# Performance work log

Measured on AMD Instinct MI355X. Metric: run time of the kernel, lower is better.

The kernel has to match this reference:

```python
import jax, jax.numpy as jnp
import numpy as np

B, N, C, D, K = 8, 4096, 64, 64, 16


def _knn_indices(features, k):
    # so topk-smallest indices match torch.cdist + topk(largest=False))
    sq = jnp.sum(features * features, axis=-1)                      # [B, N]
    d2 = sq[:, :, None] + sq[:, None, :] - 2.0 * jnp.einsum('bic,bjc->bij', features, features)
    n = features.shape[1]
    eye = jnp.eye(n, dtype=bool)[None]                              # mask self
    d2 = jnp.where(eye, jnp.inf, d2)
    _, idx = jax.lax.top_k(-d2, k)                                  # k smallest
    return idx                                                      # [B, N, k]


def setup_inputs() -> dict:
    key = jax.random.key(0)
    k0, k1, k2 = jax.random.split(key, 3)
    features = jax.random.normal(k0, (B, N, C), dtype=jnp.float32)
    W1 = jax.random.normal(k1, (2 * C, D), dtype=jnp.float32) * 0.05
    b1 = jnp.zeros((D,), dtype=jnp.float32)
    W2 = jax.random.normal(k2, (D, D), dtype=jnp.float32) * 0.05
    b2 = jnp.zeros((D,), dtype=jnp.float32)
    return {"features": features, "W1": W1, "b1": b1, "W2": W2, "b2": b2}


def reference(features, W1, b1, W2, b2):
    idx = _knn_indices(features, K)                                 # [B, N, K]
    neighbors = jax.vmap(lambda f, i: f[i])(features, idx)          # [B, N, K, C]
    central = features[:, :, None, :]                               # [B, N, 1, C]
    edge = jnp.concatenate(
        [jnp.broadcast_to(central, neighbors.shape), neighbors - central], axis=-1
    )                                                               # [B, N, K, 2C]
    h = jax.nn.gelu(edge @ W1 + b1, approximate=False)              # exact GELU (torch default)
    h = jax.nn.gelu(h @ W2 + b2, approximate=False)                 # [B, N, K, D]
    return jnp.max(h, axis=2)                                       # [B, N, D]
```

## Files before the change

kernel.cpp:

```cpp
#include <hip/hip_runtime.h>
#include <math.h>
#include <stdint.h>

#define B 8
#define N 4096
#define C 64
#define D 64
#define K 16

typedef __attribute__((ext_vector_type(8))) short short8;
typedef __attribute__((ext_vector_type(4))) float f32x4;

__device__ __forceinline__ unsigned short f2bf(float x) {
    unsigned u = __float_as_uint(x);
    unsigned r = (u + 0x7FFFu + ((u >> 16) & 1u)) >> 16;
    return (unsigned short)r;
}
__device__ __forceinline__ float bf2f(unsigned short h) {
    return __uint_as_float(((unsigned)h) << 16);
}

__device__ __forceinline__ double pack_key(float d2, unsigned idx) {
    uint2 u; u.x = idx; u.y = __float_as_uint(d2);
    return __builtin_bit_cast(double, u);
}

__global__ __launch_bounds__(256)
void prep_kernel(const float* __restrict__ F, float* __restrict__ sq,
                 unsigned short* __restrict__ HP, unsigned short* __restrict__ MP,
                 unsigned short* __restrict__ LP) {
    const int row = blockIdx.x * 256 + threadIdx.x;
    const float4* src = (const float4*)(F + (size_t)row * C);
    float4 v[16];
    #pragma unroll
    for (int q = 0; q < 16; q++) v[q] = src[q];

    {
        float r[8];
        #pragma unroll
        for (int j = 0; j < 8; j++) {
            float t = ((const float*)v)[j];
            r[j] = t * t;
        }
        #pragma unroll
        for (int m = 1; m < 8; m++) {
            #pragma unroll
            for (int j = 0; j < 8; j++) {
                float t = ((const float*)v)[8 * m + j];
                r[j] = fmaf(t, t, r[j]);
            }
        }
        sq[row] = ((r[0] + r[1]) + (r[2] + r[3])) + ((r[4] + r[5]) + (r[6] + r[7]));
    }

    uint4* dh = (uint4*)(HP + (size_t)row * C);
    uint4* dm = (uint4*)(MP + (size_t)row * C);
    uint4* dl = (uint4*)(LP + (size_t)row * C);
    #pragma unroll
    for (int c8 = 0; c8 < 8; c8++) {
        unsigned hq[4], mq[4], lq[4];
        #pragma unroll
        for (int e = 0; e < 4; e++) {
            float x0 = ((const float*)v)[c8 * 8 + 2 * e];
            float x1 = ((const float*)v)[c8 * 8 + 2 * e + 1];
            unsigned short h0 = f2bf(x0), h1 = f2bf(x1);
            float r10 = x0 - bf2f(h0), r11 = x1 - bf2f(h1);
            unsigned short m0 = f2bf(r10), m1 = f2bf(r11);
            float r20 = r10 - bf2f(m0), r21 = r11 - bf2f(m1);
            unsigned short l0 = f2bf(r20), l1 = f2bf(r21);
            hq[e] = (unsigned)h0 | ((unsigned)h1 << 16);
            mq[e] = (unsigned)m0 | ((unsigned)m1 << 16);
            lq[e] = (unsigned)l0 | ((unsigned)l1 << 16);
        }
        dh[c8] = make_uint4(hq[0], hq[1], hq[2], hq[3]);
        dm[c8] = make_uint4(mq[0], mq[1], mq[2], mq[3]);
        dl[c8] = make_uint4(lq[0], lq[1], lq[2], lq[3]);
    }
}

__device__ __forceinline__ void merge4_store(const uint64_t* __restrict__ keys,
                                             int qloc, uint64_t* __restrict__ dst) {
    const uint64_t* K0 = keys + (qloc * 4 + 0) * 16;
    const uint64_t* K1 = keys + (qloc * 4 + 1) * 16;
    const uint64_t* K2 = keys + (qloc * 4 + 2) * 16;
    const uint64_t* K3 = keys + (qloc * 4 + 3) * 16;
    int p0 = 0, p1 = 0, p2 = 0, p3 = 0;
    uint64_t h0 = K0[0], h1 = K1[0], h2 = K2[0], h3 = K3[0];
    #pragma unroll
    for (int k = 0; k < K; k++) {
        uint64_t m01 = h0 < h1 ? h0 : h1;
        uint64_t m23 = h2 < h3 ? h2 : h3;
        uint64_t mv  = m01 < m23 ? m01 : m23;
        dst[k] = mv;
        if      (mv == h0) { ++p0; h0 = (p0 < 16) ? K0[p0] : ~0ull; }
        else if (mv == h1) { ++p1; h1 = (p1 < 16) ? K1[p1] : ~0ull; }
        else if (mv == h2) { ++p2; h2 = (p2 < 16) ? K2[p2] : ~0ull; }
        else               { ++p3; h3 = (p3 < 16) ? K3[p3] : ~0ull; }
    }
}

__global__ __launch_bounds__(512, 2)
void knn_mfma_kernel(const unsigned short* __restrict__ HP,
                     const unsigned short* __restrict__ MP,
                     const unsigned short* __restrict__ LP,
                     const float* __restrict__ sqg, uint64_t* __restrict__ keysg) {
    __shared__ __align__(16) char lds[49152];

    const int s  = blockIdx.y;
    const int b  = blockIdx.z;
    const int i0 = blockIdx.x * 128;
    const int c0 = s * 2048;
    const unsigned short* Hb = HP + (size_t)b * N * C;
    const unsigned short* Mb = MP + (size_t)b * N * C;
    const unsigned short* Lb = LP + (size_t)b * N * C;
    const float* sqb = sqg + (size_t)b * N;

    const int tid = threadIdx.x;
    const int l   = tid & 63;
    const int w   = tid >> 6;

    const int lr  = tid >> 3;
    const int lq  = tid & 7;
    const int wbyte = (lr * 128 + lq * 16) ^ ((lr & 7) << 4);

    const double KMAX = __builtin_bit_cast(double, 0x7FEFFFFFFFFFFFFFull);

    uint4 ph, pm, pl;
    {
        const size_t rb = (size_t)(c0 + lr) * C + lq * 8;
        ph = *(const uint4*)(Hb + rb);
        pm = *(const uint4*)(Mb + rb);
        pl = *(const uint4*)(Lb + rb);
    }

    {
        const size_t r0 = (size_t)(i0 + lr) * C + lq * 8;
        const size_t r1 = (size_t)(i0 + 64 + lr) * C + lq * 8;
        uint4 qh0 = *(const uint4*)(Hb + r0), qh1 = *(const uint4*)(Hb + r1);
        uint4 qm0 = *(const uint4*)(Mb + r0), qm1 = *(const uint4*)(Mb + r1);
        uint4 ql0 = *(const uint4*)(Lb + r0), ql1 = *(const uint4*)(Lb + r1);
        *(uint4*)(lds +              wbyte) = qh0;
        *(uint4*)(lds +  8192      + wbyte) = qm0;
        *(uint4*)(lds + 16384      + wbyte) = ql0;
        *(uint4*)(lds + 24576      + wbyte) = qh1;
        *(uint4*)(lds + 24576+8192 + wbyte) = qm1;
        *(uint4*)(lds + 24576+16384+ wbyte) = ql1;
    }
    __syncthreads();

    const int koff = (l >> 4) * 16;
    const int swzR = (l & 7) << 4;
    const int qrow = w * 16 + (l & 15);
    const char* qbuf = lds + ((qrow >> 6) ? 24576 : 0);
    const int qr6 = qrow & 63;
    const int qb0 = (qr6 * 128 + koff) ^ swzR;
    const int qb1 = (qr6 * 128 + 64 + koff) ^ swzR;
    short8 bh0 = *(const short8*)(qbuf + qb0),         bh1 = *(const short8*)(qbuf + qb1);
    short8 bm0 = *(const short8*)(qbuf +  8192 + qb0), bm1 = *(const short8*)(qbuf +  8192 + qb1);
    short8 bl0 = *(const short8*)(qbuf + 16384 + qb0), bl1 = *(const short8*)(qbuf + 16384 + qb1);

    const float sqq   = sqb[i0 + qrow];
    const int   qglob = i0 + qrow;
    const int   crow0 = (l >> 4) * 4;
    const int   dtile = i0 + ((w >> 2) << 6);

    __syncthreads();

    *(uint4*)(lds +         wbyte) = ph;
    *(uint4*)(lds +  8192 + wbyte) = pm;
    *(uint4*)(lds + 16384 + wbyte) = pl;
    {
        const size_t rb = (size_t)(c0 + 64 + lr) * C + lq * 8;
        ph = *(const uint4*)(Hb + rb);
        pm = *(const uint4*)(Mb + rb);
        pl = *(const uint4*)(Lb + rb);
    }
    __syncthreads();

    double bd[16];
    #pragma unroll
    for (int k = 0; k < 16; k++) bd[k] = KMAX;

    for (int t = 0; t < 32; t++) {
        const int j0 = c0 + t * 64;
        char* bufA = lds + ((t & 1) ? 24576 : 0);
        char* bufB = lds + ((t & 1) ? 0 : 24576);

        if (t < 31) {
            *(uint4*)(bufB +         wbyte) = ph;
            *(uint4*)(bufB +  8192 + wbyte) = pm;
            *(uint4*)(bufB + 16384 + wbyte) = pl;
        }
        if (t < 30) {
            const size_t rb = (size_t)(j0 + 128 + lr) * C + lq * 8;
            ph = *(const uint4*)(Hb + rb);
            pm = *(const uint4*)(Mb + rb);
            pl = *(const uint4*)(Lb + rb);
        }

        float4 sqm0 = *(const float4*)(sqb + j0 +      crow0);
        float4 sqm1 = *(const float4*)(sqb + j0 + 16 + crow0);
        float4 sqm2 = *(const float4*)(sqb + j0 + 32 + crow0);
        float4 sqm3 = *(const float4*)(sqb + j0 + 48 + crow0);

        double nk[16];

        #pragma unroll
        for (int m = 0; m < 4; m++) {
            const int arow = m * 16 + (l & 15);
            const int ab0 = (arow * 128 + koff) ^ swzR;
            const int ab1 = (arow * 128 + 64 + koff) ^ swzR;
            short8 ah0 = *(const short8*)(bufA + ab0);
            short8 ah1 = *(const short8*)(bufA + ab1);
            short8 am0 = *(const short8*)(bufA + 8192 + ab0);
            short8 am1 = *(const short8*)(bufA + 8192 + ab1);
            short8 al0 = *(const short8*)(bufA + 16384 + ab0);
            short8 al1 = *(const short8*)(bufA + 16384 + ab1);

            f32x4 acc1 = {0.f, 0.f, 0.f, 0.f};
            acc1 = __builtin_amdgcn_mfma_f32_16x16x32_bf16(am0, bm0, acc1, 0, 0, 0);
            acc1 = __builtin_amdgcn_mfma_f32_16x16x32_bf16(am1, bm1, acc1, 0, 0, 0);
            acc1 = __builtin_amdgcn_mfma_f32_16x16x32_bf16(ah0, bl0, acc1, 0, 0, 0);
            acc1 = __builtin_amdgcn_mfma_f32_16x16x32_bf16(ah1, bl1, acc1, 0, 0, 0);
            acc1 = __builtin_amdgcn_mfma_f32_16x16x32_bf16(al0, bh0, acc1, 0, 0, 0);
            f32x4 acc2 = {0.f, 0.f, 0.f, 0.f};
            acc2 = __builtin_amdgcn_mfma_f32_16x16x32_bf16(al1, bh1, acc2, 0, 0, 0);
            acc2 = __builtin_amdgcn_mfma_f32_16x16x32_bf16(ah0, bm0, acc2, 0, 0, 0);
            acc2 = __builtin_amdgcn_mfma_f32_16x16x32_bf16(ah1, bm1, acc2, 0, 0, 0);
            acc2 = __builtin_amdgcn_mfma_f32_16x16x32_bf16(am0, bh0, acc2, 0, 0, 0);
            acc2 = __builtin_amdgcn_mfma_f32_16x16x32_bf16(am1, bh1, acc2, 0, 0, 0);
            f32x4 acch = {0.f, 0.f, 0.f, 0.f};
            acch = __builtin_amdgcn_mfma_f32_16x16x32_bf16(ah0, bh0, acch, 0, 0, 0);
            acch = __builtin_amdgcn_mfma_f32_16x16x32_bf16(ah1, bh1, acch, 0, 0, 0);

            float4 sqm = (m == 0) ? sqm0 : (m == 1) ? sqm1 : (m == 2) ? sqm2 : sqm3;
            #pragma unroll
            for (int r = 0; r < 4; r++) {
                float sqc = (r == 0) ? sqm.x : (r == 1) ? sqm.y : (r == 2) ? sqm.z : sqm.w;
                float gg = acch[r] + (acc1[r] + acc2[r]);
                float d2 = fmaf(-2.0f, gg, sqq + sqc);
                d2 = fmaxf(d2, 0.0f);
                nk[m * 4 + r] = pack_key(d2, (unsigned)(j0 + m * 16 + crow0 + r));
            }
        }

        if (j0 == dtile) {
            #pragma unroll
            for (int m = 0; m < 4; m++)
                #pragma unroll
                for (int r = 0; r < 4; r++)
                    if ((j0 + m * 16 + crow0 + r) == qglob) nk[m * 4 + r] = KMAX;
        }

        #pragma unroll
        for (int p = 1; p < 16; p <<= 1) {
            #pragma unroll
            for (int kk = p; kk >= 1; kk >>= 1) {
                #pragma unroll
                for (int j = kk % p; j <= 16 - 1 - kk; j += 2 * kk) {
                    #pragma unroll
                    for (int i = 0; i <= ((kk - 1 < 16 - j - kk - 1) ? kk - 1 : 16 - j - kk - 1); i++) {
                        if ((i + j) / (2 * p) == (i + j + kk) / (2 * p)) {
                            double a = nk[i + j], c2 = nk[i + j + kk];
                            nk[i + j]      = fmax(a, c2);
                            nk[i + j + kk] = fmin(a, c2);
                        }
                    }
                }
            }
        }
        #pragma unroll
        for (int i = 0; i < 16; i++) bd[i] = fmin(bd[i], nk[i]);
        #pragma unroll
        for (int j = 8; j > 0; j >>= 1) {
            #pragma unroll
            for (int i = 0; i < 16; i++) {
                int ixj = i ^ j;
                if (ixj > i) {
                    double a = bd[i], c2 = bd[ixj];
                    bd[i]   = fmin(a, c2);
                    bd[ixj] = fmax(a, c2);
                }
            }
        }

        __syncthreads();
    }

    uint64_t* keys = (uint64_t*)lds;
    if (w < 4) {
        const int qloc = w * 16 + (l & 15);
        const int base = (qloc * 4 + (l >> 4)) * 16;
        #pragma unroll
        for (int k = 0; k < 16; k++)
            keys[base + k] = __builtin_bit_cast(uint64_t, bd[k]);
    }
    __syncthreads();
    if (tid < 64)
        merge4_store(keys, tid, keysg + ((size_t)b * N + i0 + tid) * 32 + s * 16);
    __syncthreads();
    if (w >= 4) {
        const int qloc = (w - 4) * 16 + (l & 15);
        const int base = (qloc * 4 + (l >> 4)) * 16;
        #pragma unroll
        for (int k = 0; k < 16; k++)
            keys[base + k] = __builtin_bit_cast(uint64_t, bd[k]);
    }
    __syncthreads();
    if (tid < 64)
        merge4_store(keys, tid, keysg + ((size_t)b * N + i0 + 64 + tid) * 32 + s * 16);
}

__global__ __launch_bounds__(256)
void knn_merge_kernel(const uint64_t* __restrict__ keysg, int* __restrict__ knn) {
    const int q = blockIdx.x * 256 + threadIdx.x;
    const uint64_t* A  = keysg + (size_t)q * 32;
    const uint64_t* Bp = A + 16;
    int pa = 0, pb = 0;
    uint64_t ha = A[0], hb = Bp[0];
    int* dst = knn + (size_t)q * K;
    #pragma unroll
    for (int k = 0; k < K; k++) {
        uint64_t mv = ha < hb ? ha : hb;
        dst[k] = (int)(mv & 0xFFFFFFFFu);
        if (mv == ha) { ++pa; ha = (pa < 16) ? A[pa] : ~0ull; }
        else          { ++pb; hb = (pb < 16) ? Bp[pb] : ~0ull; }
    }
}

__device__ __forceinline__ float gelu_fast(float x) {
    float az = fabsf(x) * 0.70710678118654752440f;
    float t  = __builtin_amdgcn_rcpf(fmaf(0.3275911f, az, 1.0f));
    float p  = t * fmaf(t, fmaf(t, fmaf(t, fmaf(t, 1.061405429f, -1.453152027f),
                                        1.421413741f), -0.284496736f), 0.254829592f);
    float e  = p * __builtin_amdgcn_exp2f(-az * az * 1.44269504088896f);
    float g  = 0.5f * x;
    return (x >= 0.0f) ? g * (2.0f - e) : g * e;
}

#define QPW 4

__global__ __launch_bounds__(256)
void mlp_mfma_kernel(const float* __restrict__ F,
                     const unsigned short* __restrict__ HP,
                     const unsigned short* __restrict__ MP,
                     const int* __restrict__ knn,
                     const float* __restrict__ W1, const float* __restrict__ b1,
                     const float* __restrict__ W2, const float* __restrict__ b2,
                     float* __restrict__ out) {
    __shared__ __align__(16) unsigned short W1h[64 * 128];
    __shared__ __align__(16) unsigned short W1m[64 * 128];
    __shared__ __align__(16) unsigned short hbh[4][1024];
    __shared__ __align__(16) unsigned short hbm[4][1024];

    const int tid = threadIdx.x;
    const int l   = tid & 63;
    const int w   = tid >> 6;

    for (int e = tid; e < 8192; e += 256) {
        const int n = e & 63, k = e >> 6;
        const int srcrow = (k < 64) ? (64 + k) : (k - 64);
        float x = W1[srcrow * 64 + n];
        unsigned short hh = f2bf(x);
        unsigned short mm = f2bf(x - bf2f(hh));
        const int byte = (n * 256 + k * 2) ^ ((n & 15) << 4);
        *(unsigned short*)((char*)W1h + byte) = hh;
        *(unsigned short*)((char*)W1m + byte) = mm;
    }

    short8 B2h[4][2], B2m[4][2];
    float b1v[4], b2v[4];
    {
        const int n = (l & 15);
        #pragma unroll
        for (int nt = 0; nt < 4; nt++) {
            const int nn = nt * 16 + n;
            b1v[nt] = b1[nn];
            b2v[nt] = b2[nn];
            #pragma unroll
            for (int c = 0; c < 2; c++) {
                const int k0 = c * 32 + (l >> 4) * 8;
                short8 vh, vm;
                #pragma unroll
                for (int jj = 0; jj < 8; jj++) {
                    float x = W2[(k0 + jj) * 64 + nn];
                    unsigned short hh = f2bf(x);
                    vh[jj] = (short)hh;
                    vm[jj] = (short)f2bf(x - bf2f(hh));
                }
                B2h[nt][c] = vh; B2m[nt][c] = vm;
            }
        }
    }
    __syncthreads();

    const int cb   = (l >> 4) * 8;
    const int swzL = (l & 15) << 4;

    for (int jq = 0; jq < QPW; jq++) {
        const int q  = (blockIdx.x * 4 + w) * QPW + jq;
        const int b  = q >> 12;
        const int ci = q & (N - 1);
        const float*          Fb  = F  + (size_t)b * N * C;
        const unsigned short* HPb = HP + (size_t)b * N * C;
        const unsigned short* MPb = MP + (size_t)b * N * C;

        const int nb = knn[(size_t)q * K + (l & 15)];

        float4 cA0 = *(const float4*)(Fb + (size_t)ci * C + cb);
        float4 cA1 = *(const float4*)(Fb + (size_t)ci * C + cb + 4);
        float4 cB0 = *(const float4*)(Fb + (size_t)ci * C + 32 + cb);
        float4 cB1 = *(const float4*)(Fb + (size_t)ci * C + 36 + cb);
        float4 nA0 = *(const float4*)(Fb + (size_t)nb * C + cb);
        float4 nA1 = *(const float4*)(Fb + (size_t)nb * C + cb + 4);
        float4 nB0 = *(const float4*)(Fb + (size_t)nb * C + 32 + cb);
        float4 nB1 = *(const float4*)(Fb + (size_t)nb * C + 36 + cb);

        short8 ach0 = *(const short8*)(HPb + (size_t)ci * C + cb);
        short8 ach1 = *(const short8*)(HPb + (size_t)ci * C + 32 + cb);
        short8 acm0 = *(const short8*)(MPb + (size_t)ci * C + cb);
        short8 acm1 = *(const short8*)(MPb + (size_t)ci * C + 32 + cb);

        short8 adh0, adm0, adh1, adm1;
        {
            float d0[8] = {nA0.x - cA0.x, nA0.y - cA0.y, nA0.z - cA0.z, nA0.w - cA0.w,
                           nA1.x - cA1.x, nA1.y - cA1.y, nA1.z - cA1.z, nA1.w - cA1.w};
            float d1[8] = {nB0.x - cB0.x, nB0.y - cB0.y, nB0.z - cB0.z, nB0.w - cB0.w,
                           nB1.x - cB1.x, nB1.y - cB1.y, nB1.z - cB1.z, nB1.w - cB1.w};
            #pragma unroll
            for (int jj = 0; jj < 8; jj++) {
                unsigned short h0 = f2bf(d0[jj]);
                adh0[jj] = (short)h0; adm0[jj] = (short)f2bf(d0[jj] - bf2f(h0));
                unsigned short h1 = f2bf(d1[jj]);
                adh1[jj] = (short)h1; adm1[jj] = (short)f2bf(d1[jj] - bf2f(h1));
            }
        }

        #pragma unroll
        for (int nt = 0; nt < 4; nt++) {
            const int rowb = (nt * 16 + (l & 15)) * 256 + (l >> 4) * 16;
            f32x4 a1 = {0.f, 0.f, 0.f, 0.f};
            f32x4 a2 = {0.f, 0.f, 0.f, 0.f};
            #pragma unroll
            for (int kc = 0; kc < 4; kc++) {
                const int byte = (rowb + kc * 64) ^ swzL;
                short8 Bh = *(const short8*)((char*)W1h + byte);
                short8 Bm = *(const short8*)((char*)W1m + byte);
                short8 Ah = (kc == 0) ? adh0 : (kc == 1) ? adh1 : (kc == 2) ? ach0 : ach1;
                short8 Am = (kc == 0) ? adm0 : (kc == 1) ? adm1 : (kc == 2) ? acm0 : acm1;
                a1 = __builtin_amdgcn_mfma_f32_16x16x32_bf16(Ah, Bh, a1, 0, 0, 0);
                a2 = __builtin_amdgcn_mfma_f32_16x16x32_bf16(Ah, Bm, a2, 0, 0, 0);
                a2 = __builtin_amdgcn_mfma_f32_16x16x32_bf16(Am, Bh, a2, 0, 0, 0);
            }
            #pragma unroll
            for (int r = 0; r < 4; r++) {
                const int row = (l >> 4) * 4 + r;
                const int col = nt * 16 + (l & 15);
                float hv = gelu_fast(a1[r] + a2[r] + b1v[nt]);
                unsigned short hh = f2bf(hv);
                unsigned short hm = f2bf(hv - bf2f(hh));
                const int byte = (row * 128 + col * 2) ^ ((row & 7) << 4);
                *(unsigned short*)((char*)&hbh[w][0] + byte) = hh;
                *(unsigned short*)((char*)&hbm[w][0] + byte) = hm;
            }
        }

        asm volatile("s_waitcnt lgkmcnt(0)" ::: "memory");
        __builtin_amdgcn_sched_barrier(0);

        short8 Ah2[2], Am2[2];
        #pragma unroll
        for (int kc = 0; kc < 2; kc++) {
            const int byte = ((l & 15) * 128 + kc * 64 + (l >> 4) * 16) ^ (((l & 15) & 7) << 4);
            Ah2[kc] = *(const short8*)((char*)&hbh[w][0] + byte);
            Am2[kc] = *(const short8*)((char*)&hbm[w][0] + byte);
        }
        #pragma unroll
        for (int nt = 0; nt < 4; nt++) {
            f32x4 a1 = {0.f, 0.f, 0.f, 0.f};
            f32x4 a2 = {0.f, 0.f, 0.f, 0.f};
            #pragma unroll
            for (int kc = 0; kc < 2; kc++) {
                a1 = __builtin_amdgcn_mfma_f32_16x16x32_bf16(Ah2[kc], B2h[nt][kc], a1, 0, 0, 0);
                a2 = __builtin_amdgcn_mfma_f32_16x16x32_bf16(Ah2[kc], B2m[nt][kc], a2, 0, 0, 0);
                a2 = __builtin_amdgcn_mfma_f32_16x16x32_bf16(Am2[kc], B2h[nt][kc], a2, 0, 0, 0);
            }
            float mx = -INFINITY;
            #pragma unroll
            for (int r = 0; r < 4; r++)
                mx = fmaxf(mx, gelu_fast(a1[r] + a2[r] + b2v[nt]));
            mx = fmaxf(mx, __shfl_xor(mx, 16));
            mx = fmaxf(mx, __shfl_xor(mx, 32));
            if (l < 16) out[(size_t)q * D + nt * 16 + l] = mx;
        }
    }
}

extern "C" void kernel_launch(void* const* d_in, const int* in_sizes, int n_in,
                              void* d_out, int out_size, void* d_ws, size_t ws_size,
                              hipStream_t stream) {
    const float* F  = (const float*)d_in[0];
    const float* W1 = (const float*)d_in[1];
    const float* b1 = (const float*)d_in[2];
    const float* W2 = (const float*)d_in[3];
    const float* b2 = (const float*)d_in[4];
    float* out = (float*)d_out;

    char* ws = (char*)d_ws;
    float*          sq   = (float*)ws;
    uint64_t*       keys = (uint64_t*)(ws + (128 << 10));
    unsigned short* HP   = (unsigned short*)(ws + (8320 << 10));
    unsigned short* MP   = (unsigned short*)(ws + (12416 << 10));
    unsigned short* LP   = (unsigned short*)(ws + (16512 << 10));
    int*            knn  = (int*)LP;

    prep_kernel<<<dim3(B * N / 256), 256, 0, stream>>>(F, sq, HP, MP, LP);
    knn_mfma_kernel<<<dim3(N / 128, 2, B), 512, 0, stream>>>(HP, MP, LP, sq, keys);
    knn_merge_kernel<<<dim3(B * N / 256), 256, 0, stream>>>(keys, knn);
    mlp_mfma_kernel<<<dim3(B * N / (4 * QPW)), 256, 0, stream>>>(
        F, HP, MP, knn, W1, b1, W2, b2, out);
}
```

Measured before the change: 276.6 us.

## Use integer 64-bit keys for kNN sorting and prefetch neighbor rows in edge MLP

Top-k keys in the kNN kernel become packed uint64 values compared with integer compare-and-select, replacing double-precision fmin/fmax. The packed-double compares rely on FP64 min/max, while the integer version compares the same bit layout directly. Separately, the edge-MLP kernel loads all neighbor indices up front and double-buffers the neighbor feature-row loads one query ahead, so gather latency overlaps with compute. The prefetch raises register pressure, and 64-bit integer compares expand into several 32-bit instructions each.

```diff
diff --git a/kernel.cpp b/kernel.cpp
--- a/kernel.cpp
+++ b/kernel.cpp
@@ -20,10 +20,14 @@
     return __uint_as_float(((unsigned)h) << 16);
 }
 
-__device__ __forceinline__ double pack_key(float d2, unsigned idx) {
-    uint2 u; u.x = idx; u.y = __float_as_uint(d2);
-    return __builtin_bit_cast(double, u);
-}
+__device__ __forceinline__ uint64_t pack_key(float d2, unsigned idx) {
+    return ((uint64_t)__float_as_uint(d2) << 32) | idx;
+}
+
+#define CASD(A, i, j) { uint64_t _x = A[i], _y = A[j]; bool _c = _x < _y; \
+                        A[i] = _c ? _y : _x; A[j] = _c ? _x : _y; }
+#define CASA(A, i, j) { uint64_t _x = A[i], _y = A[j]; bool _c = _y < _x; \
+                        A[i] = _c ? _y : _x; A[j] = _c ? _x : _y; }
 
 __global__ __launch_bounds__(256)
 void prep_kernel(const float* __restrict__ F, float* __restrict__ sq,
@@ -122,8 +126,6 @@
     const int lr  = tid >> 3;
     const int lq  = tid & 7;
     const int wbyte = (lr * 128 + lq * 16) ^ ((lr & 7) << 4);
-
-    const double KMAX = __builtin_bit_cast(double, 0x7FEFFFFFFFFFFFFFull);
 
     uint4 ph, pm, pl;
     {
@@ -177,9 +179,9 @@
     }
     __syncthreads();
 
-    double bd[16];
-    #pragma unroll
-    for (int k = 0; k < 16; k++) bd[k] = KMAX;
+    uint64_t bd[16];
+    #pragma unroll
+    for (int k = 0; k < 16; k++) bd[k] = ~0ull;
 
     for (int t = 0; t < 32; t++) {
         const int j0 = c0 + t * 64;
@@ -203,7 +205,7 @@
         float4 sqm2 = *(const float4*)(sqb + j0 + 32 + crow0);
         float4 sqm3 = *(const float4*)(sqb + j0 + 48 + crow0);
 
-        double nk[16];
+        uint64_t nk[16];
 
         #pragma unroll
         for (int m = 0; m < 4; m++) {
@@ -249,7 +251,7 @@
             for (int m = 0; m < 4; m++)
                 #pragma unroll
                 for (int r = 0; r < 4; r++)
-                    if ((j0 + m * 16 + crow0 + r) == qglob) nk[m * 4 + r] = KMAX;
+                    if ((j0 + m * 16 + crow0 + r) == qglob) nk[m * 4 + r] = ~0ull;
         }
 
         #pragma unroll
@@ -261,25 +263,21 @@
                     #pragma unroll
                     for (int i = 0; i <= ((kk - 1 < 16 - j - kk - 1) ? kk - 1 : 16 - j - kk - 1); i++) {
                         if ((i + j) / (2 * p) == (i + j + kk) / (2 * p)) {
-                            double a = nk[i + j], c2 = nk[i + j + kk];
-                            nk[i + j]      = fmax(a, c2);
-                            nk[i + j + kk] = fmin(a, c2);
+                            CASD(nk, i + j, i + j + kk);
                         }
                     }
                 }
             }
         }
         #pragma unroll
-        for (int i = 0; i < 16; i++) bd[i] = fmin(bd[i], nk[i]);
+        for (int i = 0; i < 16; i++) bd[i] = (nk[i] < bd[i]) ? nk[i] : bd[i];
         #pragma unroll
         for (int j = 8; j > 0; j >>= 1) {
             #pragma unroll
             for (int i = 0; i < 16; i++) {
                 int ixj = i ^ j;
                 if (ixj > i) {
-                    double a = bd[i], c2 = bd[ixj];
-                    bd[i]   = fmin(a, c2);
-                    bd[ixj] = fmax(a, c2);
+                    CASA(bd, i, ixj);
                 }
             }
         }
@@ -292,8 +290,7 @@
         const int qloc = w * 16 + (l & 15);
         const int base = (qloc * 4 + (l >> 4)) * 16;
         #pragma unroll
-        for (int k = 0; k < 16; k++)
-            keys[base + k] = __builtin_bit_cast(uint64_t, bd[k]);
+        for (int k = 0; k < 16; k++) keys[base + k] = bd[k];
     }
     __syncthreads();
     if (tid < 64)
@@ -303,8 +300,7 @@
         const int qloc = (w - 4) * 16 + (l & 15);
         const int base = (qloc * 4 + (l >> 4)) * 16;
         #pragma unroll
-        for (int k = 0; k < 16; k++)
-            keys[base + k] = __builtin_bit_cast(uint64_t, bd[k]);
+        for (int k = 0; k < 16; k++) keys[base + k] = bd[k];
     }
     __syncthreads();
     if (tid < 64)
@@ -357,6 +353,15 @@
     const int l   = tid & 63;
     const int w   = tid >> 6;
 
+    const int cb   = (l >> 4) * 8;
+    const int swzL = (l & 15) << 4;
+    const int qbase = (blockIdx.x * 4 + w) * QPW;
+
+    int nbs[QPW];
+    #pragma unroll
+    for (int jq = 0; jq < QPW; jq++)
+        nbs[jq] = knn[(size_t)(qbase + jq) * K + (l & 15)];
+
     for (int e = tid; e < 8192; e += 256) {
         const int n = e & 63, k = e >> 6;
         const int srcrow = (k < 64) ? (64 + k) : (k - 64);
@@ -394,27 +399,36 @@
     }
     __syncthreads();
 
-    const int cb   = (l >> 4) * 8;
-    const int swzL = (l & 15) << 4;
-
+    float4 pnA0[2], pnA1[2], pnB0[2], pnB1[2];
+    #define LOADN(s_, jq_) { \
+        const int q_ = qbase + (jq_); \
+        const float* Fb_ = F + (size_t)(q_ >> 12) * N * C; \
+        const size_t nr_ = (size_t)nbs[jq_] * C; \
+        pnA0[s_] = *(const float4*)(Fb_ + nr_ + cb); \
+        pnA1[s_] = *(const float4*)(Fb_ + nr_ + cb + 4); \
+        pnB0[s_] = *(const float4*)(Fb_ + nr_ + 32 + cb); \
+        pnB1[s_] = *(const float4*)(Fb_ + nr_ + 36 + cb); \
+    }
+    LOADN(0, 0);
+
+    #pragma unroll
     for (int jq = 0; jq < QPW; jq++) {
-        const int q  = (blockIdx.x * 4 + w) * QPW + jq;
+        const int sbuf = jq & 1;
+        if (jq + 1 < QPW) LOADN(sbuf ^ 1, jq + 1);
+
+        const int q  = qbase + jq;
         const int b  = q >> 12;
         const int ci = q & (N - 1);
         const float*          Fb  = F  + (size_t)b * N * C;
         const unsigned short* HPb = HP + (size_t)b * N * C;
         const unsigned short* MPb = MP + (size_t)b * N * C;
 
-        const int nb = knn[(size_t)q * K + (l & 15)];
-
         float4 cA0 = *(const float4*)(Fb + (size_t)ci * C + cb);
         float4 cA1 = *(const float4*)(Fb + (size_t)ci * C + cb + 4);
         float4 cB0 = *(const float4*)(Fb + (size_t)ci * C + 32 + cb);
         float4 cB1 = *(const float4*)(Fb + (size_t)ci * C + 36 + cb);
-        float4 nA0 = *(const float4*)(Fb + (size_t)nb * C + cb);
-        float4 nA1 = *(const float4*)(Fb + (size_t)nb * C + cb + 4);
-        float4 nB0 = *(const float4*)(Fb + (size_t)nb * C + 32 + cb);
-        float4 nB1 = *(const float4*)(Fb + (size_t)nb * C + 36 + cb);
+        float4 nA0 = pnA0[sbuf], nA1 = pnA1[sbuf];
+        float4 nB0 = pnB0[sbuf], nB1 = pnB1[sbuf];
 
         short8 ach0 = *(const short8*)(HPb + (size_t)ci * C + cb);
         short8 ach1 = *(const short8*)(HPb + (size_t)ci * C + 32 + cb);
@@ -494,6 +508,7 @@
             if (l < 16) out[(size_t)q * D + nt * 16 + l] = mx;
         }
     }
+    #undef LOADN
 }
 
 extern "C" void kernel_launch(void* const* d_in, const int* in_sizes, int n_in,
```

Result: slower. 374.7 us (+35.5%).
